# Kernel optimization log

Hardware: AMD Instinct MI355X
Metric: run time of the kernel (lower is better)

The kernel has to match this reference:

```python
import jax, jax.numpy as jnp
import numpy as np

B, LATENT, HID, OUT_DIM, SEQ_LEN = 256, 64, 256, 128, 512


def setup_inputs() -> dict:
    key = jax.random.key(0)
    ks = jax.random.split(key, 9)
    s = 1.0 / np.sqrt(HID)
    return {
        "z": jax.random.normal(ks[0], (B, LATENT), dtype=jnp.float32),
        "fc_w": jax.random.normal(ks[1], (HID, LATENT), dtype=jnp.float32) * (1.0 / np.sqrt(LATENT)),
        "fc_b": jax.random.normal(ks[2], (HID,), dtype=jnp.float32) * 0.01,
        "w_ih": jax.random.normal(ks[3], (4 * HID, HID), dtype=jnp.float32) * s,
        "w_hh": jax.random.normal(ks[4], (4 * HID, HID), dtype=jnp.float32) * s,
        "b_ih": jax.random.normal(ks[5], (4 * HID,), dtype=jnp.float32) * s,
        "b_hh": jax.random.normal(ks[6], (4 * HID,), dtype=jnp.float32) * s,
        "out_w": jax.random.normal(ks[7], (OUT_DIM, HID), dtype=jnp.float32) * s,
        "out_b": jax.random.normal(ks[8], (OUT_DIM,), dtype=jnp.float32) * 0.01,
    }


def reference(z, fc_w, fc_b, w_ih, w_hh, b_ih, b_hh, out_w, out_b):
    # h0 = fc(z): [B, H]; also serves as the (time-constant) LSTM input and initial hidden state
    h0 = z @ fc_w.T + fc_b
    # Input-to-hidden projection is the same every step -> precompute once. [B, 4H]
    x_proj = h0 @ w_ih.T + (b_ih + b_hh)

    def step(carry, _):
        h, c = carry
        gates = x_proj + h @ w_hh.T  # [B, 4H]
        i, f, g, o = jnp.split(gates, 4, axis=-1)  # PyTorch gate order: i, f, g, o
        i = jax.nn.sigmoid(i)
        f = jax.nn.sigmoid(f)
        g = jnp.tanh(g)
        o = jax.nn.sigmoid(o)
        c = f * c + i * g
        h = o * jnp.tanh(c)
        return (h, c), h

    c0 = jnp.zeros_like(h0)
    _, hs = jax.lax.scan(step, (h0, c0), None, length=SEQ_LEN)  # hs: [S, B, H]
    hs = jnp.transpose(hs, (1, 0, 2))  # [B, S, H]
    return hs @ out_w.T + out_b  # [B, S, OUT_DIM]
```

## Files before the change

kernel.cpp:

```cpp
#include <hip/hip_runtime.h>
#include <hip/hip_bf16.h>


typedef __bf16 v8bf __attribute__((ext_vector_type(8)));
typedef float  v4f  __attribute__((ext_vector_type(4)));

__device__ __forceinline__ float sigmoidf_(float x) {
    return __builtin_amdgcn_rcpf(1.0f + __expf(-x));
}
__device__ __forceinline__ float tanhf_(float x) {
    float ax = fabsf(x);
    float e  = __expf(-2.0f * ax);
    float t  = (1.0f - e) * __builtin_amdgcn_rcpf(1.0f + e);
    return copysignf(t, x);
}

__global__ void cvt_kernel(const float* __restrict__ w, uint4* __restrict__ o) {
    const int gg = blockIdx.x * 256 + threadIdx.x;
    const int F = gg >> 6, l = gg & 63;
    const int wv = F >> 6, rem = F & 63;
    const int jt = rem >> 5, g4 = (rem >> 3) & 3, ks = rem & 7;
    const int row = g4 * 256 + wv * 32 + jt * 16 + (l & 15);
    const int col = ks * 32 + (l >> 4) * 8;
    const float4 a = *(const float4*)(w + row * 256 + col);
    const float4 b = *(const float4*)(w + row * 256 + col + 4);
    union { __hip_bfloat16 h[8]; uint4 u; } p;
    p.h[0] = __float2bfloat16(a.x); p.h[1] = __float2bfloat16(a.y);
    p.h[2] = __float2bfloat16(a.z); p.h[3] = __float2bfloat16(a.w);
    p.h[4] = __float2bfloat16(b.x); p.h[5] = __float2bfloat16(b.y);
    p.h[6] = __float2bfloat16(b.z); p.h[7] = __float2bfloat16(b.w);
    o[gg] = p.u;
}

constexpr int STR = 264;

__device__ constexpr int K1[4][8] = {
    {0,0,0,0, 0,0,0,0},
    {1,1,1,1, 1,1,1,1},
    {1,1,1,1, 1,2,2,2},
    {2,2,2,2, 2,2,2,2},
};
__device__ constexpr int X1[4][8] = {
    {32,33,34,35, 36,37,38,39},
    { 0, 1, 2, 3,  4, 5, 6, 7},
    { 8, 9,10,11, 12, 0, 0, 0},
    { 0, 0, 0, 0,  0, 0, 0, 0},
};

__global__ __launch_bounds__(512, 2) void lstm_main(
    const float* __restrict__ z,     const float* __restrict__ fc_w,
    const float* __restrict__ fc_b,  const float* __restrict__ w_ih,
    const float* __restrict__ b_ih,  const float* __restrict__ b_hh,
    const __hip_bfloat16* __restrict__ wbf2,
    __hip_bfloat16* __restrict__ hsb)
{
    __shared__ __align__(16) unsigned char SM[16896 + 139264];
    __hip_bfloat16* hA = (__hip_bfloat16*)SM;
    unsigned char*  WL = SM + 16896;

    const int tid  = threadIdx.x;
    const int wv   = tid >> 6;
    const int lane = tid & 63;
    const int l15  = lane & 15;
    const int quad = lane >> 4;
    const int b_base = blockIdx.x * 2;

    const int rb    = quad & 1;
    const int myjt  = quad >> 1;
    const int mycol = wv * 32 + myjt * 16 + l15;

    float* h0f = (float*)WL;
    float* xps = (float*)(WL + 16384);
    float* zt  = (float*)(WL + 81920);

    {
        if (tid < 128) zt[tid] = z[b_base * 64 + tid];
    }
    __syncthreads();

    {
        const int col = tid & 255;
        const int r   = tid >> 8;
        float a = fc_b[col];
        for (int k = 0; k < 64; k += 4) {
            const float4 w = *(const float4*)(fc_w + col * 64 + k);
            const float4 h = *(const float4*)(zt + r * 64 + k);
            a += w.x * h.x + w.y * h.y + w.z * h.z + w.w * h.w;
        }
        h0f[r * 256 + col] = a;
        hA[r * STR + col] = __float2bfloat16(a);
    }
    __syncthreads();

    {
        const int c0 = tid, c1 = tid + 512;
        float a0[2], a1[2];
        const float bb0 = b_ih[c0] + b_hh[c0];
        const float bb1 = b_ih[c1] + b_hh[c1];
        a0[0] = bb0; a0[1] = bb0; a1[0] = bb1; a1[1] = bb1;
        for (int k = 0; k < 256; k += 4) {
            const float4 w0 = *(const float4*)(w_ih + c0 * 256 + k);
            const float4 w1 = *(const float4*)(w_ih + c1 * 256 + k);
            #pragma unroll
            for (int r = 0; r < 2; ++r) {
                const float4 h = *(const float4*)(h0f + r * 256 + k);
                a0[r] += w0.x * h.x + w0.y * h.y + w0.z * h.z + w0.w * h.w;
                a1[r] += w1.x * h.x + w1.y * h.y + w1.z * h.z + w1.w * h.w;
            }
        }
        #pragma unroll
        for (int r = 0; r < 2; ++r) {
            xps[r * 1024 + c0] = a0[r];
            xps[r * 1024 + c1] = a1[r];
        }
    }
    __syncthreads();

    float xp_own[4];
    #pragma unroll
    for (int g = 0; g < 4; ++g)
        xp_own[g] = xps[rb * 1024 + g * 256 + mycol];
    __syncthreads();

    v8bf wreg[40];
    {
        const uint4* src = (const uint4*)wbf2;
        #pragma unroll
        for (int g = 0; g < 4; ++g)
            #pragma unroll
            for (int ks = 0; ks < 8; ++ks) {
                const int FR = wv * 64 + g * 8 + ks;
                union { uint4 u; v8bf v; } t; t.u = src[FR * 64 + lane];
                wreg[g * 8 + ks] = t.v;
            }
        #pragma unroll
        for (int k = 0; k < 8; ++k) {
            const int FR = wv * 64 + 32 + k;
            union { uint4 u; v8bf v; } t; t.u = src[FR * 64 + lane];
            wreg[32 + k] = t.v;
        }
        uint4* wl = (uint4*)WL;
        #pragma unroll
        for (int i = 0; i < 13; ++i) {
            const int FR = wv * 64 + 32 + 8 + i;
            wl[(wv * 13 + i) * 64 + lane] = src[FR * 64 + lane];
        }
    }

    float cst = 0.0f;
    const v4f z4 = {0.0f, 0.0f, 0.0f, 0.0f};
    const __hip_bfloat16* sbase = wbf2 + (size_t)(wv * 64 + 32) * 512 + lane * 8;
    const __hip_bfloat16* wlbase = (const __hip_bfloat16*)WL + (size_t)(wv * 13) * 512 + lane * 8;
    __hip_bfloat16* hsp = hsb + (size_t)(b_base + rb) * 131072 + mycol;

    __syncthreads();

    for (int t = 0; t < 512; ++t) {
        const __hip_bfloat16* A = hA + (t & 1) * (16 * STR);
        v4f acc[2][4];

        #pragma unroll
        for (int ks = 0; ks < 8; ++ks) {
            const v8bf a = *(const v8bf*)(A + (l15 & 1) * STR + ks * 32 + quad * 8);
            #pragma unroll
            for (int g = 0; g < 4; ++g) {
                acc[0][g] = __builtin_amdgcn_mfma_f32_16x16x32_bf16(
                    a, wreg[g * 8 + ks], (ks == 0) ? z4 : acc[0][g], 0, 0, 0);
                v8bf w;
                if (K1[g][ks] == 0)      w = wreg[X1[g][ks]];
                else if (K1[g][ks] == 1) w = *(const v8bf*)(wlbase + X1[g][ks] * 512);
                else                     w = *(const v8bf*)(sbase + (g * 8 + ks) * 512);
                acc[1][g] = __builtin_amdgcn_mfma_f32_16x16x32_bf16(
                    a, w, (ks == 0) ? z4 : acc[1][g], 0, 0, 0);
            }
        }

        float gv[4];
        #pragma unroll
        for (int g = 0; g < 4; ++g) {
            const float r0 = myjt ? acc[1][g][0] : acc[0][g][0];
            const float r1 = myjt ? acc[1][g][1] : acc[0][g][1];
            gv[g] = (rb ? r1 : r0) + xp_own[g];
        }

        __hip_bfloat16* An = hA + ((t + 1) & 1) * (16 * STR);
        {
            const float iv = sigmoidf_(gv[0]);
            const float fv = sigmoidf_(gv[1]);
            const float gg = tanhf_  (gv[2]);
            const float ov = sigmoidf_(gv[3]);
            const float c  = fv * cst + iv * gg;
            cst = c;
            const __hip_bfloat16 hb = __float2bfloat16(ov * tanhf_(c));
            An[rb * STR + mycol] = hb;
            hsp[(size_t)t * 256] = hb;
        }
        asm volatile("s_waitcnt lgkmcnt(0)\n\ts_barrier" ::: "memory");
    }
}

__global__ __launch_bounds__(512, 2) void outproj_kernel(
    void* __restrict__ io, const float* __restrict__ out_w, const float* __restrict__ out_b)
{
    __shared__ __hip_bfloat16 tile[256 * STR];
    const __hip_bfloat16* hsb = (const __hip_bfloat16*)io;
    float* outp = (float*)io;

    const int tid  = threadIdx.x;
    const int wv   = tid >> 6;
    const int lane = tid & 63;
    const int l15  = lane & 15;
    const int quad = lane >> 4;
    const int m0   = blockIdx.x * 256;

    {
        const uint4* src = (const uint4*)(hsb + (size_t)m0 * 256);
        #pragma unroll
        for (int i = 0; i < 16; ++i) {
            const int cid = tid + i * 512;
            const int row = cid >> 5, c8 = (cid & 31) * 8;
            *(uint4*)&tile[row * STR + c8] = src[cid];
        }
    }
    __syncthreads();

    const int mbase = wv * 32;
    for (int nt = 0; nt < 8; ++nt) {
        union U8 { __hip_bfloat16 h[8]; v8bf v; };
        v8bf wo[8];
        #pragma unroll
        for (int ks = 0; ks < 8; ++ks) {
            const float* wr = out_w + (nt * 16 + l15) * 256 + ks * 32 + quad * 8;
            const float4 f0 = *(const float4*)wr;
            const float4 f1 = *(const float4*)(wr + 4);
            U8 u;
            u.h[0] = __float2bfloat16(f0.x); u.h[1] = __float2bfloat16(f0.y);
            u.h[2] = __float2bfloat16(f0.z); u.h[3] = __float2bfloat16(f0.w);
            u.h[4] = __float2bfloat16(f1.x); u.h[5] = __float2bfloat16(f1.y);
            u.h[6] = __float2bfloat16(f1.z); u.h[7] = __float2bfloat16(f1.w);
            wo[ks] = u.v;
        }
        const float ob = out_b[nt * 16 + l15];
        #pragma unroll
        for (int mt = 0; mt < 2; ++mt) {
            v4f oacc = { ob, ob, ob, ob };
            #pragma unroll
            for (int ks = 0; ks < 8; ++ks) {
                const v8bf a = *(const v8bf*)&tile[(mbase + mt * 16 + l15) * STR + ks * 32 + quad * 8];
                oacc = __builtin_amdgcn_mfma_f32_16x16x32_bf16(a, wo[ks], oacc, 0, 0, 0);
            }
            #pragma unroll
            for (int r = 0; r < 4; ++r)
                outp[(size_t)(m0 + mbase + mt * 16 + quad * 4 + r) * 128 + nt * 16 + l15] = oacc[r];
        }
    }
}

extern "C" void kernel_launch(void* const* d_in, const int* in_sizes, int n_in,
                              void* d_out, int out_size, void* d_ws, size_t ws_size,
                              hipStream_t stream) {
    (void)in_sizes; (void)n_in; (void)out_size; (void)ws_size;
    const float* z     = (const float*)d_in[0];
    const float* fc_w  = (const float*)d_in[1];
    const float* fc_b  = (const float*)d_in[2];
    const float* w_ih  = (const float*)d_in[3];
    const float* w_hh  = (const float*)d_in[4];
    const float* b_ih  = (const float*)d_in[5];
    const float* b_hh  = (const float*)d_in[6];
    const float* out_w = (const float*)d_in[7];
    const float* out_b = (const float*)d_in[8];

    __hip_bfloat16* wbf2 = (__hip_bfloat16*)d_ws;

    hipLaunchKernelGGL(cvt_kernel, dim3(128), dim3(256), 0, stream, w_hh, (uint4*)wbf2);
    hipLaunchKernelGGL(lstm_main,  dim3(128), dim3(512), 0, stream,
                       z, fc_w, fc_b, w_ih, b_ih, b_hh, wbf2, (__hip_bfloat16*)d_out);
    hipLaunchKernelGGL(outproj_kernel, dim3(512), dim3(512), 0, stream,
                       d_out, out_w, out_b);
}
```

Measured before the change: 838.2 us.

## Keep more W_hh fragments in registers and pre-convert out_w to bf16 fragments

In the recurrent kernel, four more bf16 W_hh MFMA fragments per wave move from LDS into registers (wreg grows from 40 to 44), and the LDS-resident set shrinks from 13 to 9 fragments. This cuts LDS reads on the serial 512-step critical path, at the cost of higher register pressure and possible spills. The output projection now reads out_w already converted to bf16 in fragment layout by a new small conversion kernel, instead of converting fp32 on the fly in every block. It also uses 128-row tiles with twice as many blocks and a higher occupancy hint.

```diff
diff --git a/kernel.cpp b/kernel.cpp
--- a/kernel.cpp
+++ b/kernel.cpp
@@ -32,18 +32,34 @@
     o[gg] = p.u;
 }
 
+__global__ void cvt_ow(const float* __restrict__ w, uint4* __restrict__ o) {
+    const int gg = blockIdx.x * 256 + threadIdx.x;
+    const int F = gg >> 6, l = gg & 63;
+    const int nt = F >> 3, ks = F & 7;
+    const int row = nt * 16 + (l & 15);
+    const int col = ks * 32 + (l >> 4) * 8;
+    const float4 a = *(const float4*)(w + row * 256 + col);
+    const float4 b = *(const float4*)(w + row * 256 + col + 4);
+    union { __hip_bfloat16 h[8]; uint4 u; } p;
+    p.h[0] = __float2bfloat16(a.x); p.h[1] = __float2bfloat16(a.y);
+    p.h[2] = __float2bfloat16(a.z); p.h[3] = __float2bfloat16(a.w);
+    p.h[4] = __float2bfloat16(b.x); p.h[5] = __float2bfloat16(b.y);
+    p.h[6] = __float2bfloat16(b.z); p.h[7] = __float2bfloat16(b.w);
+    o[gg] = p.u;
+}
+
 constexpr int STR = 264;
 
 __device__ constexpr int K1[4][8] = {
     {0,0,0,0, 0,0,0,0},
-    {1,1,1,1, 1,1,1,1},
+    {0,0,0,0, 1,1,1,1},
     {1,1,1,1, 1,2,2,2},
     {2,2,2,2, 2,2,2,2},
 };
 __device__ constexpr int X1[4][8] = {
     {32,33,34,35, 36,37,38,39},
-    { 0, 1, 2, 3,  4, 5, 6, 7},
-    { 8, 9,10,11, 12, 0, 0, 0},
+    {40,41,42,43,  0, 1, 2, 3},
+    { 4, 5, 6, 7,  8, 0, 0, 0},
     { 0, 0, 0, 0,  0, 0, 0, 0},
 };
 
@@ -122,7 +138,7 @@
         xp_own[g] = xps[rb * 1024 + g * 256 + mycol];
     __syncthreads();
 
-    v8bf wreg[40];
+    v8bf wreg[44];
     {
         const uint4* src = (const uint4*)wbf2;
         #pragma unroll
@@ -134,23 +150,23 @@
                 wreg[g * 8 + ks] = t.v;
             }
         #pragma unroll
-        for (int k = 0; k < 8; ++k) {
+        for (int k = 0; k < 12; ++k) {
             const int FR = wv * 64 + 32 + k;
             union { uint4 u; v8bf v; } t; t.u = src[FR * 64 + lane];
             wreg[32 + k] = t.v;
         }
         uint4* wl = (uint4*)WL;
         #pragma unroll
-        for (int i = 0; i < 13; ++i) {
-            const int FR = wv * 64 + 32 + 8 + i;
-            wl[(wv * 13 + i) * 64 + lane] = src[FR * 64 + lane];
+        for (int i = 0; i < 9; ++i) {
+            const int FR = wv * 64 + 32 + 12 + i;
+            wl[(wv * 9 + i) * 64 + lane] = src[FR * 64 + lane];
         }
     }
 
     float cst = 0.0f;
     const v4f z4 = {0.0f, 0.0f, 0.0f, 0.0f};
     const __hip_bfloat16* sbase = wbf2 + (size_t)(wv * 64 + 32) * 512 + lane * 8;
-    const __hip_bfloat16* wlbase = (const __hip_bfloat16*)WL + (size_t)(wv * 13) * 512 + lane * 8;
+    const __hip_bfloat16* wlbase = (const __hip_bfloat16*)WL + (size_t)(wv * 9) * 512 + lane * 8;
     __hip_bfloat16* hsp = hsb + (size_t)(b_base + rb) * 131072 + mycol;
 
     __syncthreads();
@@ -199,10 +215,11 @@
     }
 }
 
-__global__ __launch_bounds__(512, 2) void outproj_kernel(
-    void* __restrict__ io, const float* __restrict__ out_w, const float* __restrict__ out_b)
+__global__ __launch_bounds__(512, 4) void outproj_kernel(
+    void* __restrict__ io, const __hip_bfloat16* __restrict__ owb,
+    const float* __restrict__ out_b)
 {
-    __shared__ __hip_bfloat16 tile[256 * STR];
+    __shared__ __hip_bfloat16 tile[128 * STR];
     const __hip_bfloat16* hsb = (const __hip_bfloat16*)io;
     float* outp = (float*)io;
 
@@ -211,12 +228,12 @@
     const int lane = tid & 63;
     const int l15  = lane & 15;
     const int quad = lane >> 4;
-    const int m0   = blockIdx.x * 256;
+    const int m0   = blockIdx.x * 128;
 
     {
         const uint4* src = (const uint4*)(hsb + (size_t)m0 * 256);
         #pragma unroll
-        for (int i = 0; i < 16; ++i) {
+        for (int i = 0; i < 8; ++i) {
             const int cid = tid + i * 512;
             const int row = cid >> 5, c8 = (cid & 31) * 8;
             *(uint4*)&tile[row * STR + c8] = src[cid];
@@ -224,35 +241,23 @@
     }
     __syncthreads();
 
-    const int mbase = wv * 32;
+    const int mbase = wv * 16;
+    const __hip_bfloat16* wob = owb + lane * 8;
     for (int nt = 0; nt < 8; ++nt) {
-        union U8 { __hip_bfloat16 h[8]; v8bf v; };
         v8bf wo[8];
         #pragma unroll
+        for (int ks = 0; ks < 8; ++ks)
+            wo[ks] = *(const v8bf*)(wob + (size_t)(nt * 8 + ks) * 512);
+        const float ob = out_b[nt * 16 + l15];
+        v4f oacc = { ob, ob, ob, ob };
+        #pragma unroll
         for (int ks = 0; ks < 8; ++ks) {
-            const float* wr = out_w + (nt * 16 + l15) * 256 + ks * 32 + quad * 8;
-            const float4 f0 = *(const float4*)wr;
-            const float4 f1 = *(const float4*)(wr + 4);
-            U8 u;
-            u.h[0] = __float2bfloat16(f0.x); u.h[1] = __float2bfloat16(f0.y);
-            u.h[2] = __float2bfloat16(f0.z); u.h[3] = __float2bfloat16(f0.w);
-            u.h[4] = __float2bfloat16(f1.x); u.h[5] = __float2bfloat16(f1.y);
-            u.h[6] = __float2bfloat16(f1.z); u.h[7] = __float2bfloat16(f1.w);
-            wo[ks] = u.v;
-        }
-        const float ob = out_b[nt * 16 + l15];
-        #pragma unroll
-        for (int mt = 0; mt < 2; ++mt) {
-            v4f oacc = { ob, ob, ob, ob };
-            #pragma unroll
-            for (int ks = 0; ks < 8; ++ks) {
-                const v8bf a = *(const v8bf*)&tile[(mbase + mt * 16 + l15) * STR + ks * 32 + quad * 8];
-                oacc = __builtin_amdgcn_mfma_f32_16x16x32_bf16(a, wo[ks], oacc, 0, 0, 0);
-            }
-            #pragma unroll
-            for (int r = 0; r < 4; ++r)
-                outp[(size_t)(m0 + mbase + mt * 16 + quad * 4 + r) * 128 + nt * 16 + l15] = oacc[r];
-        }
+            const v8bf a = *(const v8bf*)&tile[(mbase + l15) * STR + ks * 32 + quad * 8];
+            oacc = __builtin_amdgcn_mfma_f32_16x16x32_bf16(a, wo[ks], oacc, 0, 0, 0);
+        }
+        #pragma unroll
+        for (int r = 0; r < 4; ++r)
+            outp[(size_t)(m0 + mbase + quad * 4 + r) * 128 + nt * 16 + l15] = oacc[r];
     }
 }
 
@@ -271,10 +276,12 @@
     const float* out_b = (const float*)d_in[8];
 
     __hip_bfloat16* wbf2 = (__hip_bfloat16*)d_ws;
+    __hip_bfloat16* owb  = (__hip_bfloat16*)d_ws + 262144;
 
     hipLaunchKernelGGL(cvt_kernel, dim3(128), dim3(256), 0, stream, w_hh, (uint4*)wbf2);
+    hipLaunchKernelGGL(cvt_ow,     dim3(16),  dim3(256), 0, stream, out_w, (uint4*)owb);
     hipLaunchKernelGGL(lstm_main,  dim3(128), dim3(512), 0, stream,
                        z, fc_w, fc_b, w_ih, b_ih, b_hh, wbf2, (__hip_bfloat16*)d_out);
-    hipLaunchKernelGGL(outproj_kernel, dim3(512), dim3(512), 0, stream,
-                       d_out, out_w, out_b);
-}
+    hipLaunchKernelGGL(outproj_kernel, dim3(1024), dim3(512), 0, stream,
+                       d_out, owb, out_b);
+}
```

Result: slower. 948.4 us (+13.1%).
